# Kernel optimization log

Hardware: AMD Instinct MI355X
Metric: run time of the kernel (lower is better)

## Reference

```python
import jax, jax.numpy as jnp
import numpy as np

TEMP = 2.0   # NTXent uses a hardcoded temperature of 2, not the ctor's 0.07
EPS = 1e-8   # F.cosine_similarity eps


def setup_inputs() -> dict:
    key = jax.random.key(0)
    k1, _ = jax.random.split(key)
    x = jax.random.normal(k1, (8192, 256), dtype=jnp.float32)
    unused = jnp.zeros((1,), dtype=jnp.int32)
    return {"x": x, "unused": unused}


def _cos_matrix(a, b):
    # pairwise cosine similarity: [N, N]
    na = jnp.linalg.norm(a, axis=-1)
    nb = jnp.linalg.norm(b, axis=-1)
    dots = a @ b.T
    return dots / jnp.maximum(na[:, None] * nb[None, :], EPS)


def reference(x, unused):
    n = x.shape[0] // 2
    p, q = x[:n], x[n:]  # anchor, positive

    s_pp = _cos_matrix(p, p)
    s_pn = _cos_matrix(p, q)
    s_nn = _cos_matrix(q, q)
    s_np = _cos_matrix(q, p)

    # double loop i, j in [i, n): upper triangle including diagonal
    mask = jnp.triu(jnp.ones((n, n), dtype=bool))

    exp_sum = (jnp.exp(s_pp / TEMP) + jnp.exp(s_pn / TEMP)
               + jnp.exp(s_nn / TEMP) + jnp.exp(s_np / TEMP))
    sim_all = jnp.sum(jnp.where(mask, exp_sum, 0.0))

    sim_s = jnp.sum(jnp.exp(jnp.diagonal(s_pn) / TEMP))

    return -jnp.log(sim_s / sim_all)
```

## Files before the change

### kernel.cpp

```cpp
#include <hip/hip_runtime.h>

#define DIM     256
#define NROWS   8192
#define NTILE   64
#define NBLK    ((NTILE * (NTILE + 1)) / 2)
#define GB      1040
#define NPART   (GB * 4)
#define CHPLANE ((size_t)NROWS * 16)

using i32x4  = __attribute__((ext_vector_type(4))) int;
using i32x8  = __attribute__((ext_vector_type(8))) int;
using f32x16 = __attribute__((ext_vector_type(16))) float;

struct i32x8_pair { i32x4 lo, hi; };

__device__ __forceinline__ unsigned fp4q(float v) {
  float a = fabsf(v);
  unsigned s = (__builtin_bit_cast(unsigned, v) >> 31) << 3;
  unsigned c = a < 0.25f ? 0u : a < 0.75f ? 1u : a < 1.25f ? 2u : a < 1.75f ? 3u
             : a < 2.50f ? 4u : a < 3.50f ? 5u : a < 5.00f ? 6u : 7u;
  return s | c;
}

__device__ __forceinline__ void tile_rc(int t, int& bi, int& bj) {
  int i = (int)((129.0 - sqrt(129.0 * 129.0 - 8.0 * (double)t)) * 0.5);
  while ((i * (129 - i)) / 2 > t) --i;
  while (((i + 1) * (128 - i)) / 2 <= t) ++i;
  bi = i;
  bj = i + (t - (i * (129 - i)) / 2);
}

__device__ __forceinline__ float exp_half(float x) {
  float t = x * 0.7213475204444817f;
  float r;
  asm("v_exp_f32 %0, %1" : "=v"(r) : "v"(t));
  return r;
}

__global__ __launch_bounds__(256) void normalize_k(const float* __restrict__ x,
                                                   unsigned char* __restrict__ z4) {
  const int w    = threadIdx.x >> 6;
  const int lane = threadIdx.x & 63;
  const int row0 = blockIdx.x * 32 + w * 8;
#pragma unroll
  for (int r = 0; r < 8; ++r) {
    const int row = row0 + r;
    float4 v = ((const float4*)(x + (size_t)row * DIM))[lane];
    float ss = v.x * v.x + v.y * v.y + v.z * v.z + v.w * v.w;
#pragma unroll
    for (int off = 32; off > 0; off >>= 1) ss += __shfl_xor(ss, off, 64);
    float rn = rsqrtf(fmaxf(ss, 1e-24f)) * 16.0f;
    unsigned c0 = fp4q(v.x * rn), c1 = fp4q(v.y * rn);
    unsigned c2 = fp4q(v.z * rn), c3 = fp4q(v.w * rn);
    unsigned short pk = (unsigned short)((c0 | (c1 << 4)) | ((c2 | (c3 << 4)) << 8));
    *(unsigned short*)(z4 + (size_t)(lane >> 3) * CHPLANE
                          + (size_t)row * 16 + ((2 * lane) & 14)) = pk;
  }
}

__global__ __launch_bounds__(256, 4) void gram_k(const unsigned char* __restrict__ z4,
                                                 double2* __restrict__ partial) {
  const int tid   = threadIdx.x;
  const int lane  = tid & 63;
  const int w     = tid >> 6;
  const int wr    = w >> 1, wc = w & 1;
  const int l31   = lane & 31;
  const int khalf = lane >> 5;

  double accS = 0.0, accD = 0.0;
  const i32x4 zero4 = {0, 0, 0, 0};

  for (int k = 0; k < 2; ++k) {
    int bi, bj; tile_rc(blockIdx.x * 2 + k, bi, bj);

    const unsigned char* baseA = z4 + (size_t)khalf * CHPLANE
                               + ((size_t)bi * 128 + wr * 64 + l31) * 16;
    const unsigned char* baseB = z4 + (size_t)khalf * CHPLANE
                               + ((size_t)bj * 128 + wc * 64 + l31) * 16;

    f32x16 acc_f[2][2] = {};
#pragma unroll
    for (int kc = 0; kc < 4; ++kc) {
      i32x8 a[2], b[2];
#pragma unroll
      for (int t = 0; t < 2; ++t) {
        i32x8_pair pa = { *(const i32x4*)(baseA + (size_t)(2 * kc) * CHPLANE + t * 512),
                          zero4 };
        a[t] = __builtin_bit_cast(i32x8, pa);
        i32x8_pair pb = { *(const i32x4*)(baseB + (size_t)(2 * kc) * CHPLANE + t * 512),
                          zero4 };
        b[t] = __builtin_bit_cast(i32x8, pb);
      }
#pragma unroll
      for (int ti = 0; ti < 2; ++ti)
#pragma unroll
        for (int tj = 0; tj < 2; ++tj)
          acc_f[ti][tj] = __builtin_amdgcn_mfma_scale_f32_32x32x64_f8f6f4(
              a[ti], b[tj], acc_f[ti][tj],
              4, 4,
              0, 0x7B7B7B7B,
              0, 0x7B7B7B7B);
    }

    const bool tdiag = (bi == bj);
    const bool sdiag = (bj == bi + 32);
    float ls[4] = {0.f, 0.f, 0.f, 0.f};
    float dsum = 0.0f;
    if (tdiag || sdiag) {
#pragma unroll
      for (int ti = 0; ti < 2; ++ti)
#pragma unroll
        for (int tj = 0; tj < 2; ++tj)
#pragma unroll
          for (int r = 0; r < 16; ++r) {
            float e = exp_half(acc_f[ti][tj][r]);
            ls[r & 3] += e;
            int row_l = (r & 3) + 8 * (r >> 2) + 4 * khalf;
            if (wr == wc && ti == tj && row_l == l31) dsum += e;
          }
    } else {
#pragma unroll
      for (int ti = 0; ti < 2; ++ti)
#pragma unroll
        for (int tj = 0; tj < 2; ++tj)
#pragma unroll
          for (int r = 0; r < 16; ++r)
            ls[r & 3] += exp_half(acc_f[ti][tj][r]);
    }
    float lsum = (ls[0] + ls[1]) + (ls[2] + ls[3]);
    accS += tdiag ? (double)lsum + (double)dsum : 2.0 * (double)lsum;
    if (sdiag) accD += (double)dsum;
  }

#pragma unroll
  for (int off = 32; off > 0; off >>= 1) {
    accS += __shfl_xor(accS, off, 64);
    accD += __shfl_xor(accD, off, 64);
  }
  if (lane == 0) {
    double2 v; v.x = accS; v.y = accD;
    partial[blockIdx.x * 4 + w] = v;
  }
}

__global__ __launch_bounds__(256) void reduce_k(const double2* __restrict__ partial,
                                               float* __restrict__ out) {
  __shared__ double redS[4], redD[4];
  double s = 0.0, ss = 0.0;
  for (int i = threadIdx.x; i < NPART; i += 256) {
    double2 v = partial[i];
    s += v.x; ss += v.y;
  }
#pragma unroll
  for (int off = 32; off > 0; off >>= 1) {
    s  += __shfl_xor(s,  off, 64);
    ss += __shfl_xor(ss, off, 64);
  }
  const int w = threadIdx.x >> 6;
  if ((threadIdx.x & 63) == 0) { redS[w] = s; redD[w] = ss; }
  __syncthreads();
  if (threadIdx.x == 0) {
    double S  = redS[0] + redS[1] + redS[2] + redS[3];
    double sd = redD[0] + redD[1] + redD[2] + redD[3];
    out[0] = (float)(log(0.5 * S + sd) - log(sd));
  }
}

extern "C" void kernel_launch(void* const* d_in, const int* in_sizes, int n_in,
                              void* d_out, int out_size, void* d_ws, size_t ws_size,
                              hipStream_t stream) {
  const float* x    = (const float*)d_in[0];
  unsigned char* z4 = (unsigned char*)d_ws;
  double2* partial  = (double2*)((char*)d_ws + 8 * CHPLANE);
  float* out        = (float*)d_out;

  normalize_k<<<dim3(256),  dim3(256), 0, stream>>>(x, z4);
  gram_k<<<dim3(GB),        dim3(256), 0, stream>>>(z4, partial);
  reduce_k<<<dim3(1),       dim3(256), 0, stream>>>(partial, out);
}
```

Measured before the change: 82.07 us.

## Fuse final reduction into gram kernel via atomic last-block detection

Removes the separate single-block reduce kernel: each gram block reduces its four waves in shared memory, writes one partial, and increments one of eight group counters; the last-arriving group's finisher block sums all partials and writes the loss. Gram now runs one tile per block (2080 blocks) instead of two, with launch bounds lowered to 3 blocks per SIMD, and normalize uses one row per wave over more blocks while zeroing the counters. This removes one kernel launch and gap. In exchange it adds atomic traffic and a serial tail reduction inside the last block.

```diff
diff --git a/kernel.cpp b/kernel.cpp
--- a/kernel.cpp
+++ b/kernel.cpp
@@ -4,9 +4,9 @@
 #define NROWS   8192
 #define NTILE   64
 #define NBLK    ((NTILE * (NTILE + 1)) / 2)
-#define GB      1040
-#define NPART   (GB * 4)
+#define GSZ     (NBLK / 8)
 #define CHPLANE ((size_t)NROWS * 16)
+#define CNTW    (9 * 32)
 
 using i32x4  = __attribute__((ext_vector_type(4))) int;
 using i32x8  = __attribute__((ext_vector_type(8))) int;
@@ -38,28 +38,32 @@
 }
 
 __global__ __launch_bounds__(256) void normalize_k(const float* __restrict__ x,
-                                                   unsigned char* __restrict__ z4) {
-  const int w    = threadIdx.x >> 6;
+                                                   unsigned char* __restrict__ z4,
+                                                   unsigned int* __restrict__ cnt) {
+  if (blockIdx.x == 0) {
+    for (int i = threadIdx.x; i < CNTW; i += 256) cnt[i] = 0u;
+  }
+  const int row  = blockIdx.x * 4 + (threadIdx.x >> 6);
   const int lane = threadIdx.x & 63;
-  const int row0 = blockIdx.x * 32 + w * 8;
+  float4 v = ((const float4*)(x + (size_t)row * DIM))[lane];
+  float ss = v.x * v.x + v.y * v.y + v.z * v.z + v.w * v.w;
 #pragma unroll
-  for (int r = 0; r < 8; ++r) {
-    const int row = row0 + r;
-    float4 v = ((const float4*)(x + (size_t)row * DIM))[lane];
-    float ss = v.x * v.x + v.y * v.y + v.z * v.z + v.w * v.w;
-#pragma unroll
-    for (int off = 32; off > 0; off >>= 1) ss += __shfl_xor(ss, off, 64);
-    float rn = rsqrtf(fmaxf(ss, 1e-24f)) * 16.0f;
-    unsigned c0 = fp4q(v.x * rn), c1 = fp4q(v.y * rn);
-    unsigned c2 = fp4q(v.z * rn), c3 = fp4q(v.w * rn);
-    unsigned short pk = (unsigned short)((c0 | (c1 << 4)) | ((c2 | (c3 << 4)) << 8));
-    *(unsigned short*)(z4 + (size_t)(lane >> 3) * CHPLANE
-                          + (size_t)row * 16 + ((2 * lane) & 14)) = pk;
-  }
+  for (int off = 32; off > 0; off >>= 1) ss += __shfl_xor(ss, off, 64);
+  float rn = rsqrtf(fmaxf(ss, 1e-24f)) * 16.0f;
+  unsigned c0 = fp4q(v.x * rn), c1 = fp4q(v.y * rn);
+  unsigned c2 = fp4q(v.z * rn), c3 = fp4q(v.w * rn);
+  unsigned short pk = (unsigned short)((c0 | (c1 << 4)) | ((c2 | (c3 << 4)) << 8));
+  *(unsigned short*)(z4 + (size_t)(lane >> 3) * CHPLANE
+                        + (size_t)row * 16 + ((2 * lane) & 14)) = pk;
 }
 
-__global__ __launch_bounds__(256, 4) void gram_k(const unsigned char* __restrict__ z4,
-                                                 double2* __restrict__ partial) {
+__global__ __launch_bounds__(256, 3) void gram_k(const unsigned char* __restrict__ z4,
+                                                 double2* __restrict__ partial,
+                                                 unsigned int* __restrict__ cnt,
+                                                 float* __restrict__ out) {
+  __shared__ double redS[4], redD[4];
+  __shared__ int sflag;
+
   const int tid   = threadIdx.x;
   const int lane  = tid & 63;
   const int w     = tid >> 6;
@@ -67,102 +71,110 @@
   const int l31   = lane & 31;
   const int khalf = lane >> 5;
 
-  double accS = 0.0, accD = 0.0;
+  int bi, bj; tile_rc(blockIdx.x, bi, bj);
+
+  const unsigned char* baseA = z4 + (size_t)khalf * CHPLANE
+                             + ((size_t)bi * 128 + wr * 64 + l31) * 16;
+  const unsigned char* baseB = z4 + (size_t)khalf * CHPLANE
+                             + ((size_t)bj * 128 + wc * 64 + l31) * 16;
+
+  f32x16 acc_f[2][2] = {};
   const i32x4 zero4 = {0, 0, 0, 0};
-
-  for (int k = 0; k < 2; ++k) {
-    int bi, bj; tile_rc(blockIdx.x * 2 + k, bi, bj);
-
-    const unsigned char* baseA = z4 + (size_t)khalf * CHPLANE
-                               + ((size_t)bi * 128 + wr * 64 + l31) * 16;
-    const unsigned char* baseB = z4 + (size_t)khalf * CHPLANE
-                               + ((size_t)bj * 128 + wc * 64 + l31) * 16;
-
-    f32x16 acc_f[2][2] = {};
 #pragma unroll
-    for (int kc = 0; kc < 4; ++kc) {
-      i32x8 a[2], b[2];
+  for (int kc = 0; kc < 4; ++kc) {
+    i32x8 a[2], b[2];
 #pragma unroll
-      for (int t = 0; t < 2; ++t) {
-        i32x8_pair pa = { *(const i32x4*)(baseA + (size_t)(2 * kc) * CHPLANE + t * 512),
-                          zero4 };
-        a[t] = __builtin_bit_cast(i32x8, pa);
-        i32x8_pair pb = { *(const i32x4*)(baseB + (size_t)(2 * kc) * CHPLANE + t * 512),
-                          zero4 };
-        b[t] = __builtin_bit_cast(i32x8, pb);
-      }
+    for (int t = 0; t < 2; ++t) {
+      i32x8_pair pa = { *(const i32x4*)(baseA + (size_t)(2 * kc) * CHPLANE + t * 512),
+                        zero4 };
+      a[t] = __builtin_bit_cast(i32x8, pa);
+      i32x8_pair pb = { *(const i32x4*)(baseB + (size_t)(2 * kc) * CHPLANE + t * 512),
+                        zero4 };
+      b[t] = __builtin_bit_cast(i32x8, pb);
+    }
 #pragma unroll
-      for (int ti = 0; ti < 2; ++ti)
+    for (int ti = 0; ti < 2; ++ti)
 #pragma unroll
-        for (int tj = 0; tj < 2; ++tj)
-          acc_f[ti][tj] = __builtin_amdgcn_mfma_scale_f32_32x32x64_f8f6f4(
-              a[ti], b[tj], acc_f[ti][tj],
-              4, 4,
-              0, 0x7B7B7B7B,
-              0, 0x7B7B7B7B);
-    }
-
-    const bool tdiag = (bi == bj);
-    const bool sdiag = (bj == bi + 32);
-    float ls[4] = {0.f, 0.f, 0.f, 0.f};
-    float dsum = 0.0f;
-    if (tdiag || sdiag) {
-#pragma unroll
-      for (int ti = 0; ti < 2; ++ti)
-#pragma unroll
-        for (int tj = 0; tj < 2; ++tj)
-#pragma unroll
-          for (int r = 0; r < 16; ++r) {
-            float e = exp_half(acc_f[ti][tj][r]);
-            ls[r & 3] += e;
-            int row_l = (r & 3) + 8 * (r >> 2) + 4 * khalf;
-            if (wr == wc && ti == tj && row_l == l31) dsum += e;
-          }
-    } else {
-#pragma unroll
-      for (int ti = 0; ti < 2; ++ti)
-#pragma unroll
-        for (int tj = 0; tj < 2; ++tj)
-#pragma unroll
-          for (int r = 0; r < 16; ++r)
-            ls[r & 3] += exp_half(acc_f[ti][tj][r]);
-    }
-    float lsum = (ls[0] + ls[1]) + (ls[2] + ls[3]);
-    accS += tdiag ? (double)lsum + (double)dsum : 2.0 * (double)lsum;
-    if (sdiag) accD += (double)dsum;
+      for (int tj = 0; tj < 2; ++tj)
+        acc_f[ti][tj] = __builtin_amdgcn_mfma_scale_f32_32x32x64_f8f6f4(
+            a[ti], b[tj], acc_f[ti][tj],
+            4, 4,
+            0, 0x7B7B7B7B,
+            0, 0x7B7B7B7B);
   }
 
+  const bool tdiag = (bi == bj);
+  const bool sdiag = (bj == bi + 32);
+  float ls[4] = {0.f, 0.f, 0.f, 0.f};
+  float dsum = 0.0f;
+  if (tdiag || sdiag) {
+#pragma unroll
+    for (int ti = 0; ti < 2; ++ti)
+#pragma unroll
+      for (int tj = 0; tj < 2; ++tj)
+#pragma unroll
+        for (int r = 0; r < 16; ++r) {
+          float e = exp_half(acc_f[ti][tj][r]);
+          ls[r & 3] += e;
+          int row_l = (r & 3) + 8 * (r >> 2) + 4 * khalf;
+          if (wr == wc && ti == tj && row_l == l31) dsum += e;
+        }
+  } else {
+#pragma unroll
+    for (int ti = 0; ti < 2; ++ti)
+#pragma unroll
+      for (int tj = 0; tj < 2; ++tj)
+#pragma unroll
+        for (int r = 0; r < 16; ++r)
+          ls[r & 3] += exp_half(acc_f[ti][tj][r]);
+  }
+  float lsum = (ls[0] + ls[1]) + (ls[2] + ls[3]);
+  double aS = tdiag ? (double)lsum + (double)dsum : 2.0 * (double)lsum;
+  double aD = sdiag ? (double)dsum : 0.0;
 #pragma unroll
   for (int off = 32; off > 0; off >>= 1) {
-    accS += __shfl_xor(accS, off, 64);
-    accD += __shfl_xor(accD, off, 64);
+    aS += __shfl_xor(aS, off, 64);
+    aD += __shfl_xor(aD, off, 64);
   }
-  if (lane == 0) {
-    double2 v; v.x = accS; v.y = accD;
-    partial[blockIdx.x * 4 + w] = v;
+  if (lane == 0) { redS[w] = aS; redD[w] = aD; }
+  __syncthreads();
+
+  if (tid == 0) {
+    double2 v;
+    v.x = (redS[0] + redS[1]) + (redS[2] + redS[3]);
+    v.y = (redD[0] + redD[1]) + (redD[2] + redD[3]);
+    partial[blockIdx.x] = v;
+    int last = 0;
+    unsigned g = (unsigned)(blockIdx.x & 7) * 32;
+    unsigned og = __hip_atomic_fetch_add(&cnt[g], 1u, __ATOMIC_ACQ_REL,
+                                         __HIP_MEMORY_SCOPE_AGENT);
+    if (og == GSZ - 1) {
+      unsigned orr = __hip_atomic_fetch_add(&cnt[8 * 32], 1u, __ATOMIC_ACQ_REL,
+                                            __HIP_MEMORY_SCOPE_AGENT);
+      if (orr == 7) last = 1;
+    }
+    sflag = last;
   }
-}
+  __syncthreads();
 
-__global__ __launch_bounds__(256) void reduce_k(const double2* __restrict__ partial,
-                                               float* __restrict__ out) {
-  __shared__ double redS[4], redD[4];
-  double s = 0.0, ss = 0.0;
-  for (int i = threadIdx.x; i < NPART; i += 256) {
-    double2 v = partial[i];
-    s += v.x; ss += v.y;
-  }
+  if (sflag) {
+    double s = 0.0, ss = 0.0;
+    for (int i = tid; i < NBLK; i += 256) {
+      double2 v = partial[i];
+      s += v.x; ss += v.y;
+    }
 #pragma unroll
-  for (int off = 32; off > 0; off >>= 1) {
-    s  += __shfl_xor(s,  off, 64);
-    ss += __shfl_xor(ss, off, 64);
-  }
-  const int w = threadIdx.x >> 6;
-  if ((threadIdx.x & 63) == 0) { redS[w] = s; redD[w] = ss; }
-  __syncthreads();
-  if (threadIdx.x == 0) {
-    double S  = redS[0] + redS[1] + redS[2] + redS[3];
-    double sd = redD[0] + redD[1] + redD[2] + redD[3];
-    out[0] = (float)(log(0.5 * S + sd) - log(sd));
+    for (int off = 32; off > 0; off >>= 1) {
+      s  += __shfl_xor(s,  off, 64);
+      ss += __shfl_xor(ss, off, 64);
+    }
+    if (lane == 0) { redS[w] = s; redD[w] = ss; }
+    __syncthreads();
+    if (tid == 0) {
+      double S  = (redS[0] + redS[1]) + (redS[2] + redS[3]);
+      double sd = (redD[0] + redD[1]) + (redD[2] + redD[3]);
+      out[0] = (float)(log(0.5 * S + sd) - log(sd));
+    }
   }
 }
 
@@ -172,9 +184,10 @@
   const float* x    = (const float*)d_in[0];
   unsigned char* z4 = (unsigned char*)d_ws;
   double2* partial  = (double2*)((char*)d_ws + 8 * CHPLANE);
+  unsigned int* cnt = (unsigned int*)((char*)d_ws + 8 * CHPLANE
+                                      + (size_t)NBLK * sizeof(double2));
   float* out        = (float*)d_out;
 
-  normalize_k<<<dim3(256),  dim3(256), 0, stream>>>(x, z4);
-  gram_k<<<dim3(GB),        dim3(256), 0, stream>>>(z4, partial);
-  reduce_k<<<dim3(1),       dim3(256), 0, stream>>>(partial, out);
+  normalize_k<<<dim3(NROWS / 4), dim3(256), 0, stream>>>(x, z4, cnt);
+  gram_k<<<dim3(NBLK), dim3(256), 0, stream>>>(z4, partial, cnt, out);
 }
```

Measured after the change: 101.9 us. +24.1%, slower.

## Hoist gram fragment loads, process four strided tiles per block, widen normalize grid

Applied to the files above, without the earlier changes.

The gram kernel now loads all A/B fp4 fragments for a tile before issuing the MFMAs, so memory latency overlaps better. Each block walks four tiles strided by the grid size instead of two consecutive ones. The grid is halved and the occupancy hint lowered to give more registers for the preloaded fragments. The normalize kernel now handles one row per wave across many more blocks, and a dead duplicate expression was added in fp4q.

```diff
diff --git a/kernel.cpp b/kernel.cpp
--- a/kernel.cpp
+++ b/kernel.cpp
@@ -4,7 +4,8 @@
 #define NROWS   8192
 #define NTILE   64
 #define NBLK    ((NTILE * (NTILE + 1)) / 2)
-#define GB      1040
+#define GB      520
+#define TPB     4
 #define NPART   (GB * 4)
 #define CHPLANE ((size_t)NROWS * 16)
 
@@ -18,7 +19,9 @@
   float a = fabsf(v);
   unsigned s = (__builtin_bit_cast(unsigned, v) >> 31) << 3;
   unsigned c = a < 0.25f ? 0u : a < 0.75f ? 1u : a < 1.25f ? 2u : a < 1.75f ? 3u
-             : a < 2.50f ? 4u : a < 3.50f ? 5u : a < 5.00f ? 6u : 7u;
+             : a < 2.50f ? 4u : a < 3.50f ? 5u : a < 7u;
+  c = a < 0.25f ? 0u : a < 0.75f ? 1u : a < 1.25f ? 2u : a < 1.75f ? 3u
+    : a < 2.50f ? 4u : a < 3.50f ? 5u : a < 5.00f ? 6u : 7u;
   return s | c;
 }
 
@@ -39,26 +42,21 @@
 
 __global__ __launch_bounds__(256) void normalize_k(const float* __restrict__ x,
                                                    unsigned char* __restrict__ z4) {
-  const int w    = threadIdx.x >> 6;
+  const int row  = blockIdx.x * 4 + (threadIdx.x >> 6);
   const int lane = threadIdx.x & 63;
-  const int row0 = blockIdx.x * 32 + w * 8;
+  float4 v = ((const float4*)(x + (size_t)row * DIM))[lane];
+  float ss = v.x * v.x + v.y * v.y + v.z * v.z + v.w * v.w;
 #pragma unroll
-  for (int r = 0; r < 8; ++r) {
-    const int row = row0 + r;
-    float4 v = ((const float4*)(x + (size_t)row * DIM))[lane];
-    float ss = v.x * v.x + v.y * v.y + v.z * v.z + v.w * v.w;
-#pragma unroll
-    for (int off = 32; off > 0; off >>= 1) ss += __shfl_xor(ss, off, 64);
-    float rn = rsqrtf(fmaxf(ss, 1e-24f)) * 16.0f;
-    unsigned c0 = fp4q(v.x * rn), c1 = fp4q(v.y * rn);
-    unsigned c2 = fp4q(v.z * rn), c3 = fp4q(v.w * rn);
-    unsigned short pk = (unsigned short)((c0 | (c1 << 4)) | ((c2 | (c3 << 4)) << 8));
-    *(unsigned short*)(z4 + (size_t)(lane >> 3) * CHPLANE
-                          + (size_t)row * 16 + ((2 * lane) & 14)) = pk;
-  }
+  for (int off = 32; off > 0; off >>= 1) ss += __shfl_xor(ss, off, 64);
+  float rn = rsqrtf(fmaxf(ss, 1e-24f)) * 16.0f;
+  unsigned c0 = fp4q(v.x * rn), c1 = fp4q(v.y * rn);
+  unsigned c2 = fp4q(v.z * rn), c3 = fp4q(v.w * rn);
+  unsigned short pk = (unsigned short)((c0 | (c1 << 4)) | ((c2 | (c3 << 4)) << 8));
+  *(unsigned short*)(z4 + (size_t)(lane >> 3) * CHPLANE
+                        + (size_t)row * 16 + ((2 * lane) & 14)) = pk;
 }
 
-__global__ __launch_bounds__(256, 4) void gram_k(const unsigned char* __restrict__ z4,
+__global__ __launch_bounds__(256, 2) void gram_k(const unsigned char* __restrict__ z4,
                                                  double2* __restrict__ partial) {
   const int tid   = threadIdx.x;
   const int lane  = tid & 63;
@@ -70,36 +68,40 @@
   double accS = 0.0, accD = 0.0;
   const i32x4 zero4 = {0, 0, 0, 0};
 
-  for (int k = 0; k < 2; ++k) {
-    int bi, bj; tile_rc(blockIdx.x * 2 + k, bi, bj);
+#pragma unroll 1
+  for (int k = 0; k < TPB; ++k) {
+    int bi, bj; tile_rc(blockIdx.x + k * GB, bi, bj);
 
     const unsigned char* baseA = z4 + (size_t)khalf * CHPLANE
                                + ((size_t)bi * 128 + wr * 64 + l31) * 16;
     const unsigned char* baseB = z4 + (size_t)khalf * CHPLANE
                                + ((size_t)bj * 128 + wc * 64 + l31) * 16;
 
+    i32x4 af[4][2], bf[4][2];
+#pragma unroll
+    for (int kc = 0; kc < 4; ++kc)
+#pragma unroll
+      for (int t = 0; t < 2; ++t) {
+        af[kc][t] = *(const i32x4*)(baseA + (size_t)(2 * kc) * CHPLANE + t * 512);
+        bf[kc][t] = *(const i32x4*)(baseB + (size_t)(2 * kc) * CHPLANE + t * 512);
+      }
+
     f32x16 acc_f[2][2] = {};
 #pragma unroll
     for (int kc = 0; kc < 4; ++kc) {
-      i32x8 a[2], b[2];
-#pragma unroll
-      for (int t = 0; t < 2; ++t) {
-        i32x8_pair pa = { *(const i32x4*)(baseA + (size_t)(2 * kc) * CHPLANE + t * 512),
-                          zero4 };
-        a[t] = __builtin_bit_cast(i32x8, pa);
-        i32x8_pair pb = { *(const i32x4*)(baseB + (size_t)(2 * kc) * CHPLANE + t * 512),
-                          zero4 };
-        b[t] = __builtin_bit_cast(i32x8, pb);
-      }
 #pragma unroll
       for (int ti = 0; ti < 2; ++ti)
 #pragma unroll
-        for (int tj = 0; tj < 2; ++tj)
+        for (int tj = 0; tj < 2; ++tj) {
+          i32x8_pair pa = { af[kc][ti], zero4 };
+          i32x8_pair pb = { bf[kc][tj], zero4 };
           acc_f[ti][tj] = __builtin_amdgcn_mfma_scale_f32_32x32x64_f8f6f4(
-              a[ti], b[tj], acc_f[ti][tj],
+              __builtin_bit_cast(i32x8, pa), __builtin_bit_cast(i32x8, pb),
+              acc_f[ti][tj],
               4, 4,
               0, 0x7B7B7B7B,
               0, 0x7B7B7B7B);
+        }
     }
 
     const bool tdiag = (bi == bj);
@@ -160,8 +162,8 @@
   if ((threadIdx.x & 63) == 0) { redS[w] = s; redD[w] = ss; }
   __syncthreads();
   if (threadIdx.x == 0) {
-    double S  = redS[0] + redS[1] + redS[2] + redS[3];
-    double sd = redD[0] + redD[1] + redD[2] + redD[3];
+    double S  = (redS[0] + redS[1]) + (redS[2] + redS[3]);
+    double sd = (redD[0] + redD[1]) + (redD[2] + redD[3]);
     out[0] = (float)(log(0.5 * S + sd) - log(sd));
   }
 }
@@ -174,7 +176,7 @@
   double2* partial  = (double2*)((char*)d_ws + 8 * CHPLANE);
   float* out        = (float*)d_out;
 
-  normalize_k<<<dim3(256),  dim3(256), 0, stream>>>(x, z4);
-  gram_k<<<dim3(GB),        dim3(256), 0, stream>>>(z4, partial);
-  reduce_k<<<dim3(1),       dim3(256), 0, stream>>>(partial, out);
+  normalize_k<<<dim3(NROWS / 4), dim3(256), 0, stream>>>(x, z4);
+  gram_k<<<dim3(GB), dim3(256), 0, stream>>>(z4, partial);
+  reduce_k<<<dim3(1), dim3(256), 0, stream>>>(partial, out);
 }
```

Result: faster. 75.54 us (-8.0%).
